# Optimization experiments

Measured on AMD Instinct MI355X. Metric: run time of the kernel, lower is better.

The kernel has to match this reference:

```python
import jax, jax.numpy as jnp
import numpy as np

B, IN_SIZE, OUT_SIZE, N_QUBITS, DEPTH = 4096, 512, 256, 12, 3
C64 = jnp.complex64
BN_EPS = 1e-5


def setup_inputs() -> dict:
    key = jax.random.key(0)
    ks = jax.random.split(key, 6)
    x = jax.random.normal(ks[0], (B, IN_SIZE), jnp.float32)
    enc_w = jax.random.normal(ks[1], (N_QUBITS, IN_SIZE), jnp.float32) / np.sqrt(IN_SIZE)
    enc_b = jnp.zeros((N_QUBITS,), jnp.float32)
    rot_params = jax.random.normal(ks[2], (DEPTH, N_QUBITS, 3), jnp.float32) * 0.1
    ent_params = jax.random.normal(ks[3], (DEPTH, N_QUBITS - 1), jnp.float32) * 0.1
    dec_w = jax.random.normal(ks[4], (OUT_SIZE, N_QUBITS), jnp.float32) / np.sqrt(N_QUBITS)
    dec_b = jnp.zeros((OUT_SIZE,), jnp.float32)
    return {
        'x': x, 'enc_w': enc_w, 'enc_b': enc_b,
        'rot_params': rot_params, 'ent_params': ent_params,
        'dec_w': dec_w, 'dec_b': dec_b,
        'bn1_gamma': jnp.ones((N_QUBITS,), jnp.float32),
        'bn1_beta': jnp.zeros((N_QUBITS,), jnp.float32),
        'bn2_gamma': jnp.ones((OUT_SIZE,), jnp.float32),
        'bn2_beta': jnp.zeros((OUT_SIZE,), jnp.float32),
    }


def _m2(a, b, c, d):
    return jnp.stack([jnp.stack([a, b]), jnp.stack([c, d])]).astype(C64)


def _rx(t):
    c = jnp.cos(t / 2).astype(C64)
    s = jnp.sin(t / 2).astype(C64)
    return _m2(c, -1j * s, -1j * s, c)


def _ry(t):
    c = jnp.cos(t / 2)
    s = jnp.sin(t / 2)
    return _m2(c, -s, s, c)


def _rz(p):
    z = jnp.zeros((), C64)
    return _m2(jnp.exp(-1j * p / 2), z, z, jnp.exp(1j * p / 2))


def _apply_1q(state, U, q):
    # state: [B, 2^n]; apply 2x2 U on qubit q (qubit 0 = most significant axis)
    b = state.shape[0]
    s = state.reshape(b, 2 ** q, 2, -1)
    s = jnp.einsum('ij,bkjl->bkil', U, s)
    return s.reshape(b, -1)


def _apply_cry(state, theta, q):
    # controlled-Ry: control qubit q, target qubit q+1 (adjacent)
    b = state.shape[0]
    R = _ry(theta)
    st = state.reshape(b, 2 ** q, 2, 2, -1)
    s0 = st[:, :, 0]
    s1 = jnp.einsum('ij,bkjl->bkil', R, st[:, :, 1])
    return jnp.stack([s0, s1], axis=2).reshape(b, -1)


def _batchnorm(x, g, b):
    # BatchNorm1d in training mode: biased batch stats
    m = x.mean(0)
    v = x.var(0)
    return g * (x - m) / jnp.sqrt(v + BN_EPS) + b


def _quantum_forward(encoded, rot_params, ent_params):
    # Batched statevector simulation of the per-sample circuit.
    b, n = encoded.shape
    depth = rot_params.shape[0]
    # amplitude encoding: normalize, theta = 2*arcsin(clip(|a|,0,1)), P(pi) if a<0
    norm = jnp.linalg.norm(encoded, axis=1, keepdims=True)
    a = jnp.where(norm > 0, encoded / jnp.maximum(norm, 1e-30), encoded)
    amp = jnp.clip(jnp.abs(a), 0.0, 1.0)              # sin(theta/2)
    cos_h = jnp.sqrt(jnp.maximum(1.0 - amp * amp, 0.0))  # cos(theta/2)
    sgn = jnp.where(a < 0, -1.0, 1.0)                  # P(pi) flips sign of |1> amp
    qvec = jnp.stack([cos_h, sgn * amp], axis=-1).astype(C64)  # [B, n, 2]
    # product state via successive outer products (loop over fixed n qubits)
    state = jnp.ones((b, 1), C64)
    for q in range(n):
        state = (state[:, :, None] * qvec[:, q, None, :]).reshape(b, -1)
    # parameterized circuit
    for l in range(depth):
        for q in range(n):
            U = _rz(rot_params[l, q, 2]) @ _ry(rot_params[l, q, 1]) @ _rx(rot_params[l, q, 0])
            state = _apply_1q(state, U, q)
        for q in range(n - 1):
            state = _apply_cry(state, ent_params[l, q], q)
    # per-qubit P(|1>) measurement probabilities
    idx = jnp.arange(2 ** n)
    bits = ((idx[:, None] >> (n - 1 - jnp.arange(n))) & 1).astype(jnp.float32)  # [2^n, n]
    probs = (jnp.abs(state) ** 2).astype(jnp.float32) @ bits  # [B, n]
    return probs


def reference(x, enc_w, enc_b, rot_params, ent_params, dec_w, dec_b,
              bn1_gamma, bn1_beta, bn2_gamma, bn2_beta):
    encoded = x @ enc_w.T + enc_b
    encoded = jnp.tanh(_batchnorm(encoded, bn1_gamma, bn1_beta))
    probs = _quantum_forward(encoded, rot_params, ent_params)
    out = probs @ dec_w.T + dec_b
    return _batchnorm(out, bn2_gamma, bn2_beta)
```

## Files before the change

kernel.cpp:

```cpp
#include <hip/hip_runtime.h>

#define BATCH   4096
#define IN_SZ   512
#define NQ      12
#define OUT_SZ  256
#define DEPTH   3
#define NST     4096
#define BN_EPS  1e-5f

#define OFF_ENC    0
#define OFF_BN1M   49152
#define OFF_BN1R   49168
#define OFF_GU     49184
#define OFF_GC     49472
#define OFF_PROBS  49568
#define OFF_ACC    98720

typedef float v2f __attribute__((ext_vector_type(2)));
typedef float v4f __attribute__((ext_vector_type(4)));
#define SW2(a) __builtin_shufflevector(a, a, 1, 0)

__global__ void k_encode(const float* __restrict__ x, const float* __restrict__ w,
                         const float* __restrict__ bvec,
                         const float* __restrict__ rot, const float* __restrict__ ent,
                         float* __restrict__ enc, float* __restrict__ gU, float* __restrict__ gC,
                         float* __restrict__ accum) {
    if (blockIdx.x == 1024) {
        int t = threadIdx.x;
        if (t < 90) accum[t] = 0.f;
        if (t < DEPTH * NQ) {
            float ax = rot[t * 3 + 0] * 0.5f;
            float ay = rot[t * 3 + 1] * 0.5f;
            float az = rot[t * 3 + 2] * 0.5f;
            float cx = cosf(ax), sx = sinf(ax);
            float cy = cosf(ay), sy = sinf(ay);
            float cz = cosf(az), sz = sinf(az);
            float m00r =  cy * cx, m00i =  sy * sx;
            float m01r = -sy * cx, m01i = -cy * sx;
            float m10r =  sy * cx, m10i = -cy * sx;
            float m11r =  cy * cx, m11i = -sy * sx;
            float* o = gU + t * 8;
            o[0] = cz * m00r + sz * m00i;  o[1] = cz * m00i - sz * m00r;
            o[2] = cz * m01r + sz * m01i;  o[3] = cz * m01i - sz * m01r;
            o[4] = cz * m10r - sz * m10i;  o[5] = cz * m10i + sz * m10r;
            o[6] = cz * m11r - sz * m11i;  o[7] = cz * m11i + sz * m11r;
        }
        if (t >= 128 && t - 128 < DEPTH * (NQ - 1)) {
            int i = t - 128;
            float th = ent[i] * 0.5f;
            gC[i * 2 + 0] = cosf(th);
            gC[i * 2 + 1] = sinf(th);
        }
        return;
    }
    int t = threadIdx.x;
    int wv = t >> 6, lane = t & 63;
    int row = blockIdx.x * 4 + wv;
    const float4* xr = (const float4*)(x + row * IN_SZ) + lane * 2;
    float4 xa = xr[0], xb = xr[1];
    float acc[NQ];
    #pragma unroll
    for (int q = 0; q < NQ; q++) {
        const float4* wr = (const float4*)(w + q * IN_SZ) + lane * 2;
        float4 wa = wr[0], wb = wr[1];
        float d = xa.x*wa.x + xa.y*wa.y + xa.z*wa.z + xa.w*wa.w
                + xb.x*wb.x + xb.y*wb.y + xb.z*wb.z + xb.w*wb.w;
        #pragma unroll
        for (int o = 32; o > 0; o >>= 1) d += __shfl_down(d, o, 64);
        acc[q] = d;
    }
    if (lane == 0) {
        float* er = enc + row * NQ;
        #pragma unroll
        for (int q = 0; q < NQ; q++) er[q] = acc[q] + bvec[q];
    }
}

__global__ void k_bnstats(const float* __restrict__ xm, float* __restrict__ mo,
                          float* __restrict__ ro) {
    __shared__ float scr[32];
    int j = blockIdx.x, t = threadIdx.x;
    float s = 0.f, s2 = 0.f;
    for (int b = t; b < BATCH; b += 1024) {
        float v = xm[b * NQ + j];
        s += v; s2 += v * v;
    }
    #pragma unroll
    for (int o = 32; o > 0; o >>= 1) { s += __shfl_down(s, o, 64); s2 += __shfl_down(s2, o, 64); }
    int lane = t & 63, w = t >> 6;
    if (lane == 0) { scr[w] = s; scr[16 + w] = s2; }
    __syncthreads();
    if (t == 0) {
        float S = 0.f, S2 = 0.f;
        #pragma unroll
        for (int i = 0; i < 16; i++) { S += scr[i]; S2 += scr[16 + i]; }
        float mean = S / (float)BATCH;
        float var  = S2 / (float)BATCH - mean * mean;
        mo[j] = mean;
        ro[j] = 1.f / sqrtf(var + BN_EPS);
    }
}

#define SLA2(j) ((T << 4) | ((((j) ^ ((T >> 1) & 7))) << 1))
#define SLB(m)  (((T & 0xF0) << 4) | ((m) << 4) | ((T & 15) ^ ((m) & 14)))
#define SLC(m)  (((m) << 8) | (T ^ ((((T >> 5) & 7)) << 1)))

#define LDA(j, Ra, Rb) { v4f t_ = *(const v4f*)(xch + SLA2(j));                 \
    Ra = __builtin_shufflevector(t_, t_, 0, 1);                                 \
    Rb = __builtin_shufflevector(t_, t_, 2, 3); }
#define STA(j, Ra, Rb) { v4f t_ = __builtin_shufflevector(Ra, Rb, 0, 1, 2, 3);  \
    *(v4f*)(xch + SLA2(j)) = t_; }

#define LOADA do { LDA(0,s0,s1) LDA(1,s2,s3) LDA(2,s4,s5) LDA(3,s6,s7)          \
    LDA(4,s8,s9) LDA(5,s10,s11) LDA(6,s12,s13) LDA(7,s14,s15) } while (0)
#define STORA do { STA(0,s0,s1) STA(1,s2,s3) STA(2,s4,s5) STA(3,s6,s7)          \
    STA(4,s8,s9) STA(5,s10,s11) STA(6,s12,s13) STA(7,s14,s15) } while (0)

#define LOADW(SL) do {                                                          \
    s0=xch[SL(0)];  s1=xch[SL(1)];  s2=xch[SL(2)];  s3=xch[SL(3)];              \
    s4=xch[SL(4)];  s5=xch[SL(5)];  s6=xch[SL(6)];  s7=xch[SL(7)];              \
    s8=xch[SL(8)];  s9=xch[SL(9)];  s10=xch[SL(10)]; s11=xch[SL(11)];           \
    s12=xch[SL(12)]; s13=xch[SL(13)]; s14=xch[SL(14)]; s15=xch[SL(15)]; } while (0)
#define STORW(SL) do {                                                          \
    xch[SL(0)]=s0;  xch[SL(1)]=s1;  xch[SL(2)]=s2;  xch[SL(3)]=s3;              \
    xch[SL(4)]=s4;  xch[SL(5)]=s5;  xch[SL(6)]=s6;  xch[SL(7)]=s7;              \
    xch[SL(8)]=s8;  xch[SL(9)]=s9;  xch[SL(10)]=s10; xch[SL(11)]=s11;           \
    xch[SL(12)]=s12; xch[SL(13)]=s13; xch[SL(14)]=s14; xch[SL(15)]=s15; } while (0)

#define U_LOADP(uptr) const float* u_ = (uptr);                                  \
    v2f c00r = {u_[0], u_[0]}, c00i = {-u_[1], u_[1]};                           \
    v2f c01r = {u_[2], u_[2]}, c01i = {-u_[3], u_[3]};                           \
    v2f c10r = {u_[4], u_[4]}, c10i = {-u_[5], u_[5]};                           \
    v2f c11r = {u_[6], u_[6]}, c11i = {-u_[7], u_[7]};

#define U_PAIRP(A, B) { v2f a0 = A, a1 = B, a0s = SW2(a0), a1s = SW2(a1);        \
    A = a0*c00r + a0s*c00i + a1*c01r + a1s*c01i;                                 \
    B = a0*c10r + a0s*c10i + a1*c11r + a1s*c11i; }

#define APPLY_U_K3(uptr) do { U_LOADP(uptr)                                      \
    U_PAIRP(s0,s8) U_PAIRP(s1,s9) U_PAIRP(s2,s10) U_PAIRP(s3,s11)                \
    U_PAIRP(s4,s12) U_PAIRP(s5,s13) U_PAIRP(s6,s14) U_PAIRP(s7,s15) } while (0)
#define APPLY_U_K2(uptr) do { U_LOADP(uptr)                                      \
    U_PAIRP(s0,s4) U_PAIRP(s1,s5) U_PAIRP(s2,s6) U_PAIRP(s3,s7)                  \
    U_PAIRP(s8,s12) U_PAIRP(s9,s13) U_PAIRP(s10,s14) U_PAIRP(s11,s15) } while (0)
#define APPLY_U_K1(uptr) do { U_LOADP(uptr)                                      \
    U_PAIRP(s0,s2) U_PAIRP(s1,s3) U_PAIRP(s4,s6) U_PAIRP(s5,s7)                  \
    U_PAIRP(s8,s10) U_PAIRP(s9,s11) U_PAIRP(s12,s14) U_PAIRP(s13,s15) } while (0)
#define APPLY_U_K0(uptr) do { U_LOADP(uptr)                                      \
    U_PAIRP(s0,s1) U_PAIRP(s2,s3) U_PAIRP(s4,s5) U_PAIRP(s6,s7)                  \
    U_PAIRP(s8,s9) U_PAIRP(s10,s11) U_PAIRP(s12,s13) U_PAIRP(s14,s15) } while (0)

#define RY_PAIRP(A, B) { v2f a0 = A, a1 = B;                                     \
    A = a0*cc2 - a1*ss2;  B = a0*ss2 + a1*cc2; }

#define CRY_32(cc, ss) do { v2f cc2 = {(cc),(cc)}, ss2 = {(ss),(ss)};            \
    RY_PAIRP(s8,s12) RY_PAIRP(s9,s13) RY_PAIRP(s10,s14) RY_PAIRP(s11,s15) } while (0)
#define CRY_21(cc, ss) do { v2f cc2 = {(cc),(cc)}, ss2 = {(ss),(ss)};            \
    RY_PAIRP(s4,s6) RY_PAIRP(s5,s7) RY_PAIRP(s12,s14) RY_PAIRP(s13,s15) } while (0)
#define CRY_10(cc, ss) do { v2f cc2 = {(cc),(cc)}, ss2 = {(ss),(ss)};            \
    RY_PAIRP(s2,s3) RY_PAIRP(s6,s7) RY_PAIRP(s10,s11) RY_PAIRP(s14,s15) } while (0)
#define RYALL_K3(cc, ss) do { v2f cc2 = {(cc),(cc)}, ss2 = {(ss),(ss)};          \
    RY_PAIRP(s0,s8) RY_PAIRP(s1,s9) RY_PAIRP(s2,s10) RY_PAIRP(s3,s11)            \
    RY_PAIRP(s4,s12) RY_PAIRP(s5,s13) RY_PAIRP(s6,s14) RY_PAIRP(s7,s15) } while (0)

#define INITJ(SR, j) { SR.x = f * (((j)&8)?qs8:qc8) * (((j)&4)?qs9:qc9)          \
    * (((j)&2)?qs10:qc10) * (((j)&1)?qs11:qc11); SR.y = 0.f; }
#define PRJ(S) ((S).x*(S).x + (S).y*(S).y)
#define WREDUCE(v) { v += __shfl_down(v,32,64); v += __shfl_down(v,16,64);       \
    v += __shfl_down(v,8,64); v += __shfl_down(v,4,64);                          \
    v += __shfl_down(v,2,64); v += __shfl_down(v,1,64); }

#define MKQ(i) float qc##i, qs##i; {                                             \
    float h_ = h##i;                                                             \
    float a_ = nz ? h_ * rinv : h_;                                              \
    float amp_ = fminf(fabsf(a_), 1.f);                                          \
    qc##i = sqrtf(fmaxf(1.f - amp_ * amp_, 0.f));                                \
    qs##i = (a_ < 0.f) ? -amp_ : amp_; }

__launch_bounds__(256)
__global__ void k_quantum(const float* __restrict__ enc,
                          const float* __restrict__ bn1m, const float* __restrict__ bn1r,
                          const float* __restrict__ g1, const float* __restrict__ b1,
                          const float* __restrict__ gU, const float* __restrict__ gC,
                          float* __restrict__ probs, float* __restrict__ accum) {
    __shared__ __align__(16) v2f xch[NST];

    int T = threadIdx.x, b = blockIdx.x;

    const float* er = enc + b * NQ;
    float h0  = tanhf(g1[0]  * (er[0]  - bn1m[0])  * bn1r[0]  + b1[0]);
    float h1  = tanhf(g1[1]  * (er[1]  - bn1m[1])  * bn1r[1]  + b1[1]);
    float h2  = tanhf(g1[2]  * (er[2]  - bn1m[2])  * bn1r[2]  + b1[2]);
    float h3  = tanhf(g1[3]  * (er[3]  - bn1m[3])  * bn1r[3]  + b1[3]);
    float h4  = tanhf(g1[4]  * (er[4]  - bn1m[4])  * bn1r[4]  + b1[4]);
    float h5  = tanhf(g1[5]  * (er[5]  - bn1m[5])  * bn1r[5]  + b1[5]);
    float h6  = tanhf(g1[6]  * (er[6]  - bn1m[6])  * bn1r[6]  + b1[6]);
    float h7  = tanhf(g1[7]  * (er[7]  - bn1m[7])  * bn1r[7]  + b1[7]);
    float h8  = tanhf(g1[8]  * (er[8]  - bn1m[8])  * bn1r[8]  + b1[8]);
    float h9  = tanhf(g1[9]  * (er[9]  - bn1m[9])  * bn1r[9]  + b1[9]);
    float h10 = tanhf(g1[10] * (er[10] - bn1m[10]) * bn1r[10] + b1[10]);
    float h11 = tanhf(g1[11] * (er[11] - bn1m[11]) * bn1r[11] + b1[11]);
    float n2 = h0*h0+h1*h1+h2*h2+h3*h3+h4*h4+h5*h5+h6*h6+h7*h7
             + h8*h8+h9*h9+h10*h10+h11*h11;
    float norm = sqrtf(n2);
    bool  nz   = norm > 0.f;
    float rinv = 1.f / fmaxf(norm, 1e-30f);
    MKQ(0) MKQ(1) MKQ(2) MKQ(3) MKQ(4) MKQ(5) MKQ(6) MKQ(7)
    MKQ(8) MKQ(9) MKQ(10) MKQ(11)

    v2f s0, s1, s2, s3, s4, s5, s6, s7, s8, s9, s10, s11, s12, s13, s14, s15;

    {
        float f = ((T>>7)&1 ? qs0 : qc0) * ((T>>6)&1 ? qs1 : qc1)
                * ((T>>5)&1 ? qs2 : qc2) * ((T>>4)&1 ? qs3 : qc3)
                * ((T>>3)&1 ? qs4 : qc4) * ((T>>2)&1 ? qs5 : qc5)
                * ((T>>1)&1 ? qs6 : qc6) * ((T>>0)&1 ? qs7 : qc7);
        INITJ(s0,0)  INITJ(s1,1)  INITJ(s2,2)  INITJ(s3,3)
        INITJ(s4,4)  INITJ(s5,5)  INITJ(s6,6)  INITJ(s7,7)
        INITJ(s8,8)  INITJ(s9,9)  INITJ(s10,10) INITJ(s11,11)
        INITJ(s12,12) INITJ(s13,13) INITJ(s14,14) INITJ(s15,15)
        APPLY_U_K3(gU + 8 * 8);
        APPLY_U_K2(gU + 9 * 8);
        APPLY_U_K1(gU + 10 * 8);
        APPLY_U_K0(gU + 11 * 8);
        STORA;
        __builtin_amdgcn_wave_barrier();
    }

    #pragma unroll 1
    for (int l = 0; l < DEPTH; l++) {
        const float* UL = gU + l * 96;
        const float* CL = gC + l * 22;
        LOADW(SLB);
        APPLY_U_K3(UL + 4 * 8);
        APPLY_U_K2(UL + 5 * 8);
        APPLY_U_K1(UL + 6 * 8);
        APPLY_U_K0(UL + 7 * 8);
        STORW(SLB);
        __syncthreads();
        LOADW(SLC);
        APPLY_U_K3(UL + 0 * 8);
        APPLY_U_K2(UL + 1 * 8);
        APPLY_U_K1(UL + 2 * 8);
        APPLY_U_K0(UL + 3 * 8);
        CRY_32(CL[0], CL[1]);
        CRY_21(CL[2], CL[3]);
        CRY_10(CL[4], CL[5]);
        STORW(SLC);
        __syncthreads();
        LOADW(SLB);
        if (T & 16) RYALL_K3(CL[6], CL[7]);
        CRY_32(CL[8], CL[9]);
        CRY_21(CL[10], CL[11]);
        CRY_10(CL[12], CL[13]);
        STORW(SLB);
        __builtin_amdgcn_wave_barrier();
        LOADA;
        if (T & 1) RYALL_K3(CL[14], CL[15]);
        CRY_32(CL[16], CL[17]);
        CRY_21(CL[18], CL[19]);
        CRY_10(CL[20], CL[21]);
        if (l < DEPTH - 1) {
            const float* UN = gU + (l + 1) * 96;
            APPLY_U_K3(UN + 8 * 8);
            APPLY_U_K2(UN + 9 * 8);
            APPLY_U_K1(UN + 10 * 8);
            APPLY_U_K0(UN + 11 * 8);
            STORA;
            __builtin_amdgcn_wave_barrier();
        }
    }

    float p0 = PRJ(s0),  p1 = PRJ(s1),  p2 = PRJ(s2),  p3 = PRJ(s3);
    float p4 = PRJ(s4),  p5 = PRJ(s5),  p6 = PRJ(s6),  p7 = PRJ(s7);
    float p8 = PRJ(s8),  p9 = PRJ(s9),  p10 = PRJ(s10), p11 = PRJ(s11);
    float p12 = PRJ(s12), p13 = PRJ(s13), p14 = PRJ(s14), p15 = PRJ(s15);
    float tot = p0+p1+p2+p3+p4+p5+p6+p7+p8+p9+p10+p11+p12+p13+p14+p15;
    float r8  = p8+p9+p10+p11+p12+p13+p14+p15;
    float r9  = p4+p5+p6+p7+p12+p13+p14+p15;
    float r10 = p2+p3+p6+p7+p10+p11+p14+p15;
    float r11 = p1+p3+p5+p7+p9+p11+p13+p15;
    float r0 = (T & 128) ? tot : 0.f;
    float r1 = (T & 64)  ? tot : 0.f;
    float r2 = (T & 32)  ? tot : 0.f;
    float r3 = (T & 16)  ? tot : 0.f;
    float r4 = (T & 8)   ? tot : 0.f;
    float r5 = (T & 4)   ? tot : 0.f;
    float r6 = (T & 2)   ? tot : 0.f;
    float r7 = (T & 1)   ? tot : 0.f;

    WREDUCE(r0) WREDUCE(r1) WREDUCE(r2) WREDUCE(r3) WREDUCE(r4) WREDUCE(r5)
    WREDUCE(r6) WREDUCE(r7) WREDUCE(r8) WREDUCE(r9) WREDUCE(r10) WREDUCE(r11)

    __syncthreads();
    float* red = (float*)xch;
    int lane = T & 63, w = T >> 6;
    if (lane == 0) {
        float* rr = red + w * NQ;
        rr[0]=r0; rr[1]=r1; rr[2]=r2; rr[3]=r3; rr[4]=r4; rr[5]=r5;
        rr[6]=r6; rr[7]=r7; rr[8]=r8; rr[9]=r9; rr[10]=r10; rr[11]=r11;
    }
    __syncthreads();
    float* pq = red + 64;
    if (T < NQ) {
        float v = red[T] + red[NQ + T] + red[2 * NQ + T] + red[3 * NQ + T];
        probs[b * NQ + T] = v;
        pq[T] = v;
    }
    __syncthreads();
    if (T < 90) {
        float v;
        if (T < NQ) {
            v = pq[T];
        } else {
            int j = T - NQ, q = 0;
            while (j >= NQ - q) { j -= NQ - q; q++; }
            v = pq[q] * pq[q + j];
        }
        unsafeAtomicAdd(accum + T, v);
    }
}

__global__ void k_final(const float* __restrict__ probs, const float* __restrict__ accum,
                        const float* __restrict__ dw,
                        const float* __restrict__ g2, const float* __restrict__ b2,
                        float* __restrict__ out) {
    __shared__ float ac[90];
    __shared__ float pm[NQ];
    __shared__ float cv[NQ * NQ];
    __shared__ float cp[2][NQ];
    int b0 = blockIdx.x * 2, t = threadIdx.x;
    if (t < 90) ac[t] = accum[t];
    __syncthreads();
    if (t < NQ) pm[t] = ac[t] * (1.f / (float)BATCH);
    __syncthreads();
    if (t < NQ * NQ) {
        int q = t / NQ, q2 = t - q * NQ;
        int lo = q < q2 ? q : q2, hi = q < q2 ? q2 : q;
        float P = ac[NQ + lo * NQ - (lo * (lo - 1)) / 2 + (hi - lo)];
        cv[t] = P * (1.f / (float)BATCH) - pm[q] * pm[q2];
    }
    if (t < NQ)                        cp[0][t]       = probs[b0 * NQ + t] - pm[t];
    else if (t >= 256 && t < 256 + NQ) cp[1][t - 256] = probs[(b0 + 1) * NQ + t - 256] - pm[t - 256];
    __syncthreads();
    int half = t >> 8, j = t & 255;
    float w[NQ];
    #pragma unroll
    for (int q = 0; q < NQ; q++) w[q] = dw[j * NQ + q];
    float var = 0.f, acc = 0.f;
    #pragma unroll
    for (int q = 0; q < NQ; q++) {
        float a = 0.f;
        #pragma unroll
        for (int q2 = 0; q2 < NQ; q2++) a += cv[q * NQ + q2] * w[q2];
        var += w[q] * a;
        acc += cp[half][q] * w[q];
    }
    out[(b0 + half) * OUT_SZ + j] = acc * (1.f / sqrtf(var + BN_EPS)) * g2[j] + b2[j];
}

extern "C" void kernel_launch(void* const* d_in, const int* in_sizes, int n_in,
                              void* d_out, int out_size, void* d_ws, size_t ws_size,
                              hipStream_t stream) {
    const float* x     = (const float*)d_in[0];
    const float* enc_w = (const float*)d_in[1];
    const float* enc_b = (const float*)d_in[2];
    const float* rot   = (const float*)d_in[3];
    const float* ent   = (const float*)d_in[4];
    const float* dec_w = (const float*)d_in[5];
    const float* g1    = (const float*)d_in[7];
    const float* b1    = (const float*)d_in[8];
    const float* g2    = (const float*)d_in[9];
    const float* b2    = (const float*)d_in[10];

    float* ws    = (float*)d_ws;
    float* enc   = ws + OFF_ENC;
    float* bn1m  = ws + OFF_BN1M;
    float* bn1r  = ws + OFF_BN1R;
    float* gU    = ws + OFF_GU;
    float* gC    = ws + OFF_GC;
    float* prb   = ws + OFF_PROBS;
    float* accum = ws + OFF_ACC;

    hipLaunchKernelGGL(k_encode, dim3(1025), dim3(256), 0, stream,
                       x, enc_w, enc_b, rot, ent, enc, gU, gC, accum);
    hipLaunchKernelGGL(k_bnstats, dim3(NQ), dim3(1024), 0, stream, enc, bn1m, bn1r);
    hipLaunchKernelGGL(k_quantum, dim3(BATCH), dim3(256), 0, stream,
                       enc, bn1m, bn1r, g1, b1, gU, gC, prb, accum);
    hipLaunchKernelGGL(k_final, dim3(BATCH / 2), dim3(512), 0, stream,
                       prb, accum, dec_w, g2, b2, (float*)d_out);
}
```

Measured before the change: 220.3 us.

## Fuse BN1 stats into encode via atomics, split decoder variance into separate kernel

Removes the k_bnstats kernel by having each encode block atomically accumulate per-qubit sums and sums of squares, which the quantum kernel then turns into mean and rstd. Atomic accumulators are padded to 32-float strides to spread contention, and they are zeroed with a memset instead of inside the kernel. The per-output variance computation (a 12x12 quadratic form) moves out of k_final into a single-block k_rstd kernel, so the 2048 final blocks no longer repeat it. This trades one kernel launch plus redundant work for extra atomics, a memset and a tiny extra kernel.

```diff
diff --git a/kernel.cpp b/kernel.cpp
--- a/kernel.cpp
+++ b/kernel.cpp
@@ -7,14 +7,16 @@
 #define DEPTH   3
 #define NST     4096
 #define BN_EPS  1e-5f
+#define INV_B   (1.f / 4096.f)
 
 #define OFF_ENC    0
-#define OFF_BN1M   49152
-#define OFF_BN1R   49168
-#define OFF_GU     49184
-#define OFF_GC     49472
-#define OFF_PROBS  49568
-#define OFF_ACC    98720
+#define OFF_GU     49152
+#define OFF_GC     49440
+#define OFF_PROBS  49536
+#define OFF_ACC24  98688
+#define OFF_ACC90  99456
+#define OFF_PMEAN  102336
+#define OFF_RSTD   102352
 
 typedef float v2f __attribute__((ext_vector_type(2)));
 typedef float v4f __attribute__((ext_vector_type(4)));
@@ -24,10 +26,9 @@
                          const float* __restrict__ bvec,
                          const float* __restrict__ rot, const float* __restrict__ ent,
                          float* __restrict__ enc, float* __restrict__ gU, float* __restrict__ gC,
-                         float* __restrict__ accum) {
+                         float* __restrict__ acc24) {
     if (blockIdx.x == 1024) {
         int t = threadIdx.x;
-        if (t < 90) accum[t] = 0.f;
         if (t < DEPTH * NQ) {
             float ax = rot[t * 3 + 0] * 0.5f;
             float ay = rot[t * 3 + 1] * 0.5f;
@@ -53,6 +54,7 @@
         }
         return;
     }
+    __shared__ float sh[4][NQ];
     int t = threadIdx.x;
     int wv = t >> 6, lane = t & 63;
     int row = blockIdx.x * 4 + wv;
@@ -72,32 +74,17 @@
     if (lane == 0) {
         float* er = enc + row * NQ;
         #pragma unroll
-        for (int q = 0; q < NQ; q++) er[q] = acc[q] + bvec[q];
-    }
-}
-
-__global__ void k_bnstats(const float* __restrict__ xm, float* __restrict__ mo,
-                          float* __restrict__ ro) {
-    __shared__ float scr[32];
-    int j = blockIdx.x, t = threadIdx.x;
-    float s = 0.f, s2 = 0.f;
-    for (int b = t; b < BATCH; b += 1024) {
-        float v = xm[b * NQ + j];
-        s += v; s2 += v * v;
-    }
-    #pragma unroll
-    for (int o = 32; o > 0; o >>= 1) { s += __shfl_down(s, o, 64); s2 += __shfl_down(s2, o, 64); }
-    int lane = t & 63, w = t >> 6;
-    if (lane == 0) { scr[w] = s; scr[16 + w] = s2; }
-    __syncthreads();
-    if (t == 0) {
-        float S = 0.f, S2 = 0.f;
-        #pragma unroll
-        for (int i = 0; i < 16; i++) { S += scr[i]; S2 += scr[16 + i]; }
-        float mean = S / (float)BATCH;
-        float var  = S2 / (float)BATCH - mean * mean;
-        mo[j] = mean;
-        ro[j] = 1.f / sqrtf(var + BN_EPS);
+        for (int q = 0; q < NQ; q++) {
+            float e = acc[q] + bvec[q];
+            er[q] = e;
+            sh[wv][q] = e;
+        }
+    }
+    __syncthreads();
+    if (t < NQ) {
+        float a = sh[0][t], bq = sh[1][t], c = sh[2][t], d = sh[3][t];
+        unsafeAtomicAdd(acc24 + t * 32,        a + bq + c + d);
+        unsafeAtomicAdd(acc24 + (NQ + t) * 32, a*a + bq*bq + c*c + d*d);
     }
 }
 
@@ -170,6 +157,12 @@
     v += __shfl_down(v,8,64); v += __shfl_down(v,4,64);                          \
     v += __shfl_down(v,2,64); v += __shfl_down(v,1,64); }
 
+#define MKH(i) float h##i; {                                                     \
+    float m_ = acc24[(i) * 32] * INV_B;                                          \
+    float v_ = acc24[(NQ + (i)) * 32] * INV_B - m_ * m_;                         \
+    float r_ = 1.f / sqrtf(v_ + BN_EPS);                                         \
+    h##i = tanhf(g1[i] * (er[i] - m_) * r_ + b1[i]); }
+
 #define MKQ(i) float qc##i, qs##i; {                                             \
     float h_ = h##i;                                                             \
     float a_ = nz ? h_ * rinv : h_;                                              \
@@ -179,27 +172,17 @@
 
 __launch_bounds__(256)
 __global__ void k_quantum(const float* __restrict__ enc,
-                          const float* __restrict__ bn1m, const float* __restrict__ bn1r,
+                          const float* __restrict__ acc24,
                           const float* __restrict__ g1, const float* __restrict__ b1,
                           const float* __restrict__ gU, const float* __restrict__ gC,
-                          float* __restrict__ probs, float* __restrict__ accum) {
+                          float* __restrict__ probs, float* __restrict__ acc90) {
     __shared__ __align__(16) v2f xch[NST];
 
     int T = threadIdx.x, b = blockIdx.x;
 
     const float* er = enc + b * NQ;
-    float h0  = tanhf(g1[0]  * (er[0]  - bn1m[0])  * bn1r[0]  + b1[0]);
-    float h1  = tanhf(g1[1]  * (er[1]  - bn1m[1])  * bn1r[1]  + b1[1]);
-    float h2  = tanhf(g1[2]  * (er[2]  - bn1m[2])  * bn1r[2]  + b1[2]);
-    float h3  = tanhf(g1[3]  * (er[3]  - bn1m[3])  * bn1r[3]  + b1[3]);
-    float h4  = tanhf(g1[4]  * (er[4]  - bn1m[4])  * bn1r[4]  + b1[4]);
-    float h5  = tanhf(g1[5]  * (er[5]  - bn1m[5])  * bn1r[5]  + b1[5]);
-    float h6  = tanhf(g1[6]  * (er[6]  - bn1m[6])  * bn1r[6]  + b1[6]);
-    float h7  = tanhf(g1[7]  * (er[7]  - bn1m[7])  * bn1r[7]  + b1[7]);
-    float h8  = tanhf(g1[8]  * (er[8]  - bn1m[8])  * bn1r[8]  + b1[8]);
-    float h9  = tanhf(g1[9]  * (er[9]  - bn1m[9])  * bn1r[9]  + b1[9]);
-    float h10 = tanhf(g1[10] * (er[10] - bn1m[10]) * bn1r[10] + b1[10]);
-    float h11 = tanhf(g1[11] * (er[11] - bn1m[11]) * bn1r[11] + b1[11]);
+    MKH(0) MKH(1) MKH(2) MKH(3) MKH(4) MKH(5) MKH(6) MKH(7)
+    MKH(8) MKH(9) MKH(10) MKH(11)
     float n2 = h0*h0+h1*h1+h2*h2+h3*h3+h4*h4+h5*h5+h6*h6+h7*h7
              + h8*h8+h9*h9+h10*h10+h11*h11;
     float norm = sqrtf(n2);
@@ -317,46 +300,57 @@
             while (j >= NQ - q) { j -= NQ - q; q++; }
             v = pq[q] * pq[q + j];
         }
-        unsafeAtomicAdd(accum + T, v);
-    }
-}
-
-__global__ void k_final(const float* __restrict__ probs, const float* __restrict__ accum,
-                        const float* __restrict__ dw,
-                        const float* __restrict__ g2, const float* __restrict__ b2,
-                        float* __restrict__ out) {
-    __shared__ float ac[90];
+        unsafeAtomicAdd(acc90 + T * 32, v);
+    }
+}
+
+__global__ void k_rstd(const float* __restrict__ acc90, const float* __restrict__ dw,
+                       float* __restrict__ pmean, float* __restrict__ rstd) {
     __shared__ float pm[NQ];
     __shared__ float cv[NQ * NQ];
-    __shared__ float cp[2][NQ];
-    int b0 = blockIdx.x * 2, t = threadIdx.x;
-    if (t < 90) ac[t] = accum[t];
-    __syncthreads();
-    if (t < NQ) pm[t] = ac[t] * (1.f / (float)BATCH);
+    int t = threadIdx.x;
+    if (t < NQ) {
+        float m = acc90[t * 32] * INV_B;
+        pm[t] = m;
+        pmean[t] = m;
+    }
     __syncthreads();
     if (t < NQ * NQ) {
         int q = t / NQ, q2 = t - q * NQ;
         int lo = q < q2 ? q : q2, hi = q < q2 ? q2 : q;
-        float P = ac[NQ + lo * NQ - (lo * (lo - 1)) / 2 + (hi - lo)];
-        cv[t] = P * (1.f / (float)BATCH) - pm[q] * pm[q2];
-    }
-    if (t < NQ)                        cp[0][t]       = probs[b0 * NQ + t] - pm[t];
-    else if (t >= 256 && t < 256 + NQ) cp[1][t - 256] = probs[(b0 + 1) * NQ + t - 256] - pm[t - 256];
-    __syncthreads();
-    int half = t >> 8, j = t & 255;
+        float P = acc90[(NQ + lo * NQ - (lo * (lo - 1)) / 2 + (hi - lo)) * 32];
+        cv[t] = P * INV_B - pm[q] * pm[q2];
+    }
+    __syncthreads();
     float w[NQ];
     #pragma unroll
-    for (int q = 0; q < NQ; q++) w[q] = dw[j * NQ + q];
-    float var = 0.f, acc = 0.f;
+    for (int q = 0; q < NQ; q++) w[q] = dw[t * NQ + q];
+    float var = 0.f;
     #pragma unroll
     for (int q = 0; q < NQ; q++) {
         float a = 0.f;
         #pragma unroll
         for (int q2 = 0; q2 < NQ; q2++) a += cv[q * NQ + q2] * w[q2];
         var += w[q] * a;
-        acc += cp[half][q] * w[q];
-    }
-    out[(b0 + half) * OUT_SZ + j] = acc * (1.f / sqrtf(var + BN_EPS)) * g2[j] + b2[j];
+    }
+    rstd[t] = 1.f / sqrtf(var + BN_EPS);
+}
+
+__global__ void k_final(const float* __restrict__ probs, const float* __restrict__ pmean,
+                        const float* __restrict__ rstd, const float* __restrict__ dw,
+                        const float* __restrict__ g2, const float* __restrict__ b2,
+                        float* __restrict__ out) {
+    __shared__ float cp[2][NQ];
+    int b0 = blockIdx.x * 2;
+    int t = threadIdx.x;
+    int half = t >> 8, j = t & 255;
+    if (t < NQ)                        cp[0][t]       = probs[b0 * NQ + t] - pmean[t];
+    else if (t >= 256 && t < 256 + NQ) cp[1][t - 256] = probs[(b0 + 1) * NQ + t - 256] - pmean[t - 256];
+    __syncthreads();
+    float acc = 0.f;
+    #pragma unroll
+    for (int q = 0; q < NQ; q++) acc += cp[half][q] * dw[j * NQ + q];
+    out[(b0 + half) * OUT_SZ + j] = acc * rstd[j] * g2[j] + b2[j];
 }
 
 extern "C" void kernel_launch(void* const* d_in, const int* in_sizes, int n_in,
@@ -375,18 +369,22 @@
 
     float* ws    = (float*)d_ws;
     float* enc   = ws + OFF_ENC;
-    float* bn1m  = ws + OFF_BN1M;
-    float* bn1r  = ws + OFF_BN1R;
     float* gU    = ws + OFF_GU;
     float* gC    = ws + OFF_GC;
     float* prb   = ws + OFF_PROBS;
-    float* accum = ws + OFF_ACC;
+    float* acc24 = ws + OFF_ACC24;
+    float* acc90 = ws + OFF_ACC90;
+    float* pmean = ws + OFF_PMEAN;
+    float* rstd  = ws + OFF_RSTD;
+
+    hipMemsetAsync(acc24, 0, (OFF_PMEAN - OFF_ACC24) * sizeof(float), stream);
 
     hipLaunchKernelGGL(k_encode, dim3(1025), dim3(256), 0, stream,
-                       x, enc_w, enc_b, rot, ent, enc, gU, gC, accum);
-    hipLaunchKernelGGL(k_bnstats, dim3(NQ), dim3(1024), 0, stream, enc, bn1m, bn1r);
+                       x, enc_w, enc_b, rot, ent, enc, gU, gC, acc24);
     hipLaunchKernelGGL(k_quantum, dim3(BATCH), dim3(256), 0, stream,
-                       enc, bn1m, bn1r, g1, b1, gU, gC, prb, accum);
+                       enc, acc24, g1, b1, gU, gC, prb, acc90);
+    hipLaunchKernelGGL(k_rstd, dim3(1), dim3(OUT_SZ), 0, stream,
+                       acc90, dec_w, pmean, rstd);
     hipLaunchKernelGGL(k_final, dim3(BATCH / 2), dim3(512), 0, stream,
-                       prb, accum, dec_w, g2, b2, (float*)d_out);
-}
+                       prb, pmean, rstd, dec_w, g2, b2, (float*)d_out);
+}
```

Result: slower. 236.1 us (+7.2%).
